# Kernel optimization log

Hardware: AMD Instinct MI355X
Metric: run time of the kernel (lower is better)

## Reference

```python
import jax, jax.numpy as jnp
import numpy as np

B, I, H, U = 2048, 512, 512, 6
NIH, IK, IV = 1, 64, 400            # input attn: heads, key/query size, value size
NCH, CK, CQ, CV = 4, 32, 32, 512    # comm attn: heads, key, query, value (CV == H required by residual add)
K = 4                               # top-k active units


def setup_inputs() -> dict:
    key = jax.random.key(0)
    ks = jax.random.split(key, 16)
    def p(k, sh, sc):
        return (sc * jax.random.normal(k, sh)).astype(jnp.float32)
    return {
        "x":  jax.random.normal(ks[0], (B, 1, I), jnp.float32),
        "hs": jax.random.normal(ks[1], (B, U, H), jnp.float32),
        "cs": jax.random.normal(ks[2], (B, U, H), jnp.float32),
        # input attention projections (nn.Linear, stored as (in,out))
        "Wk": p(ks[3], (I, NIH * IK), 0.02), "bk": jnp.zeros((NIH * IK,), jnp.float32),
        "Wv": p(ks[4], (I, NIH * IV), 0.02), "bv": jnp.zeros((NIH * IV,), jnp.float32),
        # GroupLinearLayer weights (num_blocks, din, dout), init 0.01*randn as in source
        "Wq_in": p(ks[5], (U, H, NIH * IK), 0.01),
        "Wq_c":  p(ks[6], (U, H, NCH * CQ), 0.01),
        "Wk_c":  p(ks[7], (U, H, NCH * CK), 0.01),
        "Wv_c":  p(ks[8], (U, H, NCH * CV), 0.01),
        "Wo_c":  p(ks[9], (U, NCH * CV, CV), 0.01),
        # per-unit LSTMCell params (gate order i,f,g,o)
        "W_ih": p(ks[10], (U, 4 * H, IV), 0.02),
        "W_hh": p(ks[11], (U, 4 * H, H), 0.02),
        "b_ih": jnp.zeros((U, 4 * H), jnp.float32),
        "b_hh": jnp.zeros((U, 4 * H), jnp.float32),
    }


def reference(x, hs, cs, Wk, bk, Wv, bv, Wq_in, Wq_c, Wk_c, Wv_c, Wo_c, W_ih, W_hh, b_ih, b_hh):
    b = x.shape[0]
    # append null input: (B, 2, I); column 0 = real input, column 1 = null
    x2 = jnp.concatenate([x, jnp.zeros((b, 1, I), x.dtype)], axis=1)

    # ---- input attention + top-k routing ----
    k_lay = (x2 @ Wk + bk).reshape(b, 2, NIH, IK).transpose(0, 2, 1, 3)   # (B, NIH, 2, IK)
    v_lay = (x2 @ Wv + bv).reshape(b, 2, NIH, IV).transpose(0, 2, 1, 3).mean(axis=1)  # (B, 2, IV)
    q_lay = jnp.einsum('buh,uhd->bud', hs, Wq_in).reshape(b, U, NIH, IK).transpose(0, 2, 1, 3)  # (B, NIH, U, IK)
    scores = jnp.einsum('bhud,bhnd->bhun', q_lay, k_lay) / jnp.sqrt(jnp.float32(IK))
    scores = scores.mean(axis=1)                                          # (B, U, 2)

    not_null = scores[:, :, 0]                                            # (B, U)
    _, idx = jax.lax.top_k(not_null, K)                                   # (B, K)
    mask = jnp.zeros((b, U), jnp.float32).at[jnp.arange(b)[:, None], idx].set(1.0)

    probs = jax.nn.softmax(scores, axis=-1)                               # dropout = identity (eval)
    inputs = jnp.einsum('bun,bnv->buv', probs, v_lay) * mask[:, :, None]  # (B, U, IV)

    # ---- per-unit LSTM cells (vectorized over units) ----
    gates = (jnp.einsum('buv,ugv->bug', inputs, W_ih)
             + jnp.einsum('buh,ugh->bug', hs, W_hh)
             + b_ih + b_hh)                                               # (B, U, 4H)
    i_g, f_g, g_g, o_g = jnp.split(gates, 4, axis=-1)
    c_new = jax.nn.sigmoid(f_g) * cs + jax.nn.sigmoid(i_g) * jnp.tanh(g_g)
    h_rnn = jax.nn.sigmoid(o_g) * jnp.tanh(c_new)                         # (B, U, H)

    # ---- communication attention (blocked_grad is identity in fwd) ----
    h_bg = h_rnn
    q = jnp.einsum('buh,uhd->bud', h_bg, Wq_c).reshape(b, U, NCH, CQ).transpose(0, 2, 1, 3)
    kk = jnp.einsum('buh,uhd->bud', h_bg, Wk_c).reshape(b, U, NCH, CK).transpose(0, 2, 1, 3)
    v = jnp.einsum('buh,uhd->bud', h_bg, Wv_c).reshape(b, U, NCH, CV).transpose(0, 2, 1, 3)
    att = jnp.einsum('bhud,bhnd->bhun', q, kk) / jnp.sqrt(jnp.float32(CK))  # (B, NCH, U, U)
    att = jax.nn.softmax(att, axis=-1) * mask[:, None, :, None]             # mask queries
    ctx = jnp.einsum('bhun,bhnd->bhud', att, v)                             # (B, NCH, U, CV)
    ctx = ctx.transpose(0, 2, 1, 3).reshape(b, U, NCH * CV)
    ctx = jnp.einsum('bud,udo->buo', ctx, Wo_c) + h_bg                      # residual (CV == H)

    m = mask[:, :, None]
    hs_out = m * ctx + (1.0 - m) * hs
    cs_out = m * c_new + (1.0 - m) * cs
    return (hs_out, cs_out)
```

## Files before the change

kernel.cpp:

```cpp
#include <hip/hip_runtime.h>
#include <math.h>

#define U6 6
#define BFULL 2048

typedef __bf16 bf16;
typedef __bf16 bf16x8 __attribute__((ext_vector_type(8)));
typedef float f32x4 __attribute__((ext_vector_type(4)));

__device__ __forceinline__ float sigmoidf_(float x) { return 1.0f / (1.0f + expf(-x)); }

__global__ __launch_bounds__(256) void pack_w(
    const float* __restrict__ Wk, const float* __restrict__ Wq_in,
    float* __restrict__ Wk_p, float* __restrict__ Wq_p)
{
    int idx = blockIdx.x * 256 + threadIdx.x;
    const int per = 512 * 64;
    if (idx >= 7 * per) return;
    int o = idx % per;
    int mat = idx / per;
    int j = o & 3, d = (o >> 2) & 63, kg = o >> 8;
    int k = kg * 4 + j;
    if (mat == 0) Wk_p[o] = Wk[k * 64 + d];
    else {
        int u = mat - 1;
        Wq_p[(size_t)u * per + o] = Wq_in[((size_t)u * 512 + k) * 64 + d];
    }
}

__global__ __launch_bounds__(384) void score2_kernel(
    const float* __restrict__ x, const float* __restrict__ hs,
    const float* __restrict__ Wk_p, const float* __restrict__ bk,
    const float* __restrict__ Wq_p,
    float* __restrict__ coef, float* __restrict__ maskf)
{
    __shared__ float xt[4][512];
    __shared__ float hst[4][3072];
    __shared__ float k0p[6][4][64];
    __shared__ float k0f[4][64];
    __shared__ float ss[4][6], s1s[4][6];
    const int t = threadIdx.x;
    const int u = t >> 6, d = t & 63;
    const int b4 = blockIdx.x * 4;

    for (int j = t; j < 4 * 128; j += 384)
        *(float4*)&xt[j >> 7][(j & 127) * 4] = *(const float4*)(x + (size_t)(b4 + (j >> 7)) * 512 + (j & 127) * 4);
    for (int j = t; j < 4 * 768; j += 384)
        *(float4*)&hst[j / 768][(j % 768) * 4] = *(const float4*)(hs + (size_t)(b4 + j / 768) * 3072 + (j % 768) * 4);
    __syncthreads();

    float qa[4] = {0.f, 0.f, 0.f, 0.f};
    const float4* wqp = (const float4*)(Wq_p + (size_t)u * 32768);
#pragma unroll 4
    for (int kg = 0; kg < 128; ++kg) {
        float4 w = wqp[kg * 64 + d];
#pragma unroll
        for (int b = 0; b < 4; ++b) {
            float4 h = *(const float4*)&hst[b][u * 512 + kg * 4];
            qa[b] += w.x * h.x + w.y * h.y + w.z * h.z + w.w * h.w;
        }
    }

    const int starts[6] = {0, 22, 44, 65, 86, 107};
    const int counts[6] = {22, 22, 21, 21, 21, 21};
    {
        float k0a[4] = {0.f, 0.f, 0.f, 0.f};
        const float4* wkp = (const float4*)Wk_p;
        const int st = starts[u], en = st + counts[u];
        for (int kg = st; kg < en; ++kg) {
            float4 w = wkp[kg * 64 + d];
#pragma unroll
            for (int b = 0; b < 4; ++b) {
                float4 xv = *(const float4*)&xt[b][kg * 4];
                k0a[b] += w.x * xv.x + w.y * xv.y + w.z * xv.z + w.w * xv.w;
            }
        }
#pragma unroll
        for (int b = 0; b < 4; ++b) k0p[u][b][d] = k0a[b];
    }
    __syncthreads();
    if (t < 256) {
        int b = t >> 6, dd = t & 63;
        float s = bk[dd];
#pragma unroll
        for (int uu = 0; uu < 6; ++uu) s += k0p[uu][b][dd];
        k0f[b][dd] = s;
    }
    __syncthreads();

    const float bkv = bk[d];
    float s0[4], s1[4];
#pragma unroll
    for (int b = 0; b < 4; ++b) {
        s0[b] = qa[b] * k0f[b][d];
        s1[b] = qa[b] * bkv;
    }
#pragma unroll
    for (int off = 32; off > 0; off >>= 1) {
#pragma unroll
        for (int b = 0; b < 4; ++b) {
            s0[b] += __shfl_xor(s0[b], off, 64);
            s1[b] += __shfl_xor(s1[b], off, 64);
        }
    }
    if (d == 0) {
#pragma unroll
        for (int b = 0; b < 4; ++b) { ss[b][u] = s0[b] * 0.125f; s1s[b][u] = s1[b] * 0.125f; }
    }
    __syncthreads();
    if (t < 4) {
        int bb = t;
        bool sel[6] = {false,false,false,false,false,false};
        for (int it = 0; it < 4; ++it) {
            int best = 0; float bm = -3.4e38f;
            for (int uu = 0; uu < 6; ++uu)
                if (!sel[uu] && ss[bb][uu] > bm) { bm = ss[bb][uu]; best = uu; }
            sel[best] = true;
        }
        for (int uu = 0; uu < 6; ++uu) {
            float m = sel[uu] ? 1.f : 0.f;
            float p0 = sigmoidf_(ss[bb][uu] - s1s[bb][uu]);
            maskf[(b4 + bb) * U6 + uu] = m;
            coef[(b4 + bb) * U6 + uu]  = m * p0;
        }
    }
}

__global__ __launch_bounds__(256) void build_wg(
    const float* __restrict__ Wih, const float* __restrict__ Whh,
    bf16* __restrict__ Wg)
{
    size_t idx = (size_t)blockIdx.x * 256 + threadIdx.x;
    if (idx >= 6UL * 2048 * 928) return;
    int u = (int)(idx / (2048 * 928));
    int r = (int)(idx % (2048 * 928));
    int g = r / 928, k = r - g * 928;
    float v = 0.f;
    if (k < 400)      v = Wih[((size_t)u * 2048 + g) * 400 + k];
    else if (k < 912) v = Whh[((size_t)u * 2048 + g) * 512 + (k - 400)];
    Wg[idx] = (bf16)v;
}

__global__ __launch_bounds__(256) void transpose_cvt(
    const float* __restrict__ in, bf16* __restrict__ out,
    int Kdim, int Ndim, int Nvalid, int n0base, long sInU, long sOutU)
{
    __shared__ float tile[32][33];
    const int t = threadIdx.x;
    const int c = t & 31, r8 = t >> 5;
    const int n0 = blockIdx.x * 32, k0 = blockIdx.y * 32, u = blockIdx.z;
    in  += (size_t)u * sInU;
    out += (size_t)u * sOutU;
    for (int rr = r8; rr < 32; rr += 8)
        tile[rr][c] = (n0 + c < Nvalid) ? in[(size_t)(k0 + rr) * Ndim + n0 + c] : 0.f;
    __syncthreads();
    for (int rr = r8; rr < 32; rr += 8)
        out[(size_t)(n0base + n0 + rr) * Kdim + k0 + c] = (bf16)tile[c][rr];
}

__global__ __launch_bounds__(256) void cvt16(
    const float* __restrict__ in, bf16* __restrict__ out, size_t n)
{
    size_t i = (size_t)blockIdx.x * 256 + threadIdx.x;
    if (i < n) out[i] = (bf16)in[i];
}

__global__ __launch_bounds__(256) void ag_fill(
    const float* __restrict__ hs, bf16* __restrict__ A_g)
{
    size_t idx = (size_t)blockIdx.x * 256 + threadIdx.x;
    if (idx >= (size_t)BFULL * U6 * 528) return;
    int c = (int)(idx % 528);
    size_t bu = idx / 528;
    float v = (c < 512) ? hs[bu * 512 + c] : 0.f;
    A_g[bu * 928 + 400 + c] = (bf16)v;
}

template <int EPI>
__global__ __launch_bounds__(256) void gemm_mfma(
    const bf16* __restrict__ A, int lda, long sAu,
    const bf16* __restrict__ B, long sBu,
    float* __restrict__ C, int ldc, long sCu,
    int K,
    const float* __restrict__ maskf, const float* __restrict__ hbg,
    const float* __restrict__ hs_in, float* __restrict__ out_hs, int b0)
{
    __shared__ bf16 Abuf[128 * 32];
    __shared__ bf16 Bbuf[128 * 32];
    const int t = threadIdx.x;
    const int lane = t & 63;
    const int wid = t >> 6;
    const int wr = wid >> 1, wc = wid & 1;
    const int brow0 = blockIdx.x * 128;
    const int c0 = blockIdx.y * 128;
    const int u = blockIdx.z;
    A += (size_t)u * sAu;
    B += (size_t)u * sBu;

    const int r0 = t >> 2, s0 = t & 3;
    const int r1 = r0 + 64;
    const int lo0 = r0 * 32 + ((s0 ^ ((r0 >> 1) & 3)) << 3);
    const int lo1 = r1 * 32 + ((s0 ^ ((r1 >> 1) & 3)) << 3);

    const bf16* Ap0 = A + (size_t)(brow0 + r0) * lda + s0 * 8;
    const bf16* Ap1 = A + (size_t)(brow0 + r1) * lda + s0 * 8;
    const bf16* Bp0 = B + (size_t)(c0 + r0) * K + s0 * 8;
    const bf16* Bp1 = B + (size_t)(c0 + r1) * K + s0 * 8;

    f32x4 acc[4][4];
#pragma unroll
    for (int m = 0; m < 4; ++m)
#pragma unroll
        for (int n = 0; n < 4; ++n) {
            f32x4 z = {0.f, 0.f, 0.f, 0.f};
            acc[m][n] = z;
        }

    const int nk = K >> 5;
    uint4 pa0 = *(const uint4*)(Ap0);
    uint4 pa1 = *(const uint4*)(Ap1);
    uint4 pb0 = *(const uint4*)(Bp0);
    uint4 pb1 = *(const uint4*)(Bp1);

    const int kg = lane >> 4;
    const int lr = lane & 15;

    for (int ks = 0; ks < nk; ++ks) {
        uint4 ca0 = pa0, ca1 = pa1, cb0 = pb0, cb1 = pb1;
        if (ks + 1 < nk) {
            const int kk = (ks + 1) << 5;
            pa0 = *(const uint4*)(Ap0 + kk);
            pa1 = *(const uint4*)(Ap1 + kk);
            pb0 = *(const uint4*)(Bp0 + kk);
            pb1 = *(const uint4*)(Bp1 + kk);
        }
        __syncthreads();
        *(uint4*)&Abuf[lo0] = ca0;
        *(uint4*)&Abuf[lo1] = ca1;
        *(uint4*)&Bbuf[lo0] = cb0;
        *(uint4*)&Bbuf[lo1] = cb1;
        __syncthreads();

        bf16x8 af[4], bfr[4];
#pragma unroll
        for (int m = 0; m < 4; ++m) {
            const int row = wr * 64 + m * 16 + lr;
            af[m] = *(bf16x8*)&Abuf[row * 32 + ((kg ^ ((row >> 1) & 3)) << 3)];
            const int col = wc * 64 + m * 16 + lr;
            bfr[m] = *(bf16x8*)&Bbuf[col * 32 + ((kg ^ ((col >> 1) & 3)) << 3)];
        }
#pragma unroll
        for (int m = 0; m < 4; ++m)
#pragma unroll
            for (int n = 0; n < 4; ++n)
                acc[m][n] = __builtin_amdgcn_mfma_f32_16x16x32_bf16(af[m], bfr[n], acc[m][n], 0, 0, 0);
    }

#pragma unroll
    for (int m = 0; m < 4; ++m) {
#pragma unroll
        for (int n = 0; n < 4; ++n) {
#pragma unroll
            for (int r = 0; r < 4; ++r) {
                const int row = brow0 + wr * 64 + m * 16 + kg * 4 + r;
                const int col = c0 + wc * 64 + n * 16 + lr;
                const float v = acc[m][n][r];
                if (EPI == 0) {
                    C[(size_t)u * sCu + (size_t)row * ldc + col] = v;
                } else if (EPI == 3) {
                    ((bf16*)C)[(size_t)u * sCu + (size_t)row * ldc + col] = (bf16)v;
                } else if (EPI == 2) {
                    if (col < 400) {
                        bf16* ag = (bf16*)out_hs;
                        const float bvc = hbg[col];
#pragma unroll
                        for (int uu = 0; uu < U6; ++uu) {
                            const float cf = hs_in[row * U6 + uu];
                            const float mf = maskf[row * U6 + uu];
                            ag[((size_t)row * U6 + uu) * 928 + col] = (bf16)(cf * v + mf * bvc);
                        }
                    }
                }
            }
        }
    }
}

__global__ __launch_bounds__(256) void gemm_m64_wo(
    const bf16* __restrict__ A, int lda,
    const bf16* __restrict__ B, long sBu, int K,
    const float* __restrict__ maskf, const bf16* __restrict__ h16,
    const float* __restrict__ hs_in, float* __restrict__ out_hs, int b0)
{
    __shared__ bf16 Abuf[64 * 32];
    __shared__ bf16 Bbuf[128 * 32];
    const int t = threadIdx.x;
    const int lane = t & 63;
    const int wid = t >> 6;
    const int wr = wid >> 1, wc = wid & 1;
    const int brow0 = blockIdx.x * 64;
    const int c0 = blockIdx.y * 128;
    const int u = blockIdx.z;
    B += (size_t)u * sBu;

    const int r0 = t >> 2, s0 = t & 3;
    const int r1 = r0 + 64;
    const int loA  = r0 * 32 + ((s0 ^ ((r0 >> 1) & 3)) << 3);
    const int loB0 = loA;
    const int loB1 = r1 * 32 + ((s0 ^ ((r1 >> 1) & 3)) << 3);

    const bf16* Ap  = A + (size_t)(brow0 + r0) * lda + s0 * 8;
    const bf16* Bp0 = B + (size_t)(c0 + r0) * K + s0 * 8;
    const bf16* Bp1 = B + (size_t)(c0 + r1) * K + s0 * 8;

    f32x4 acc[2][4];
#pragma unroll
    for (int m = 0; m < 2; ++m)
#pragma unroll
        for (int n = 0; n < 4; ++n) {
            f32x4 z = {0.f, 0.f, 0.f, 0.f};
            acc[m][n] = z;
        }

    const int nk = K >> 5;
    uint4 pa  = *(const uint4*)(Ap);
    uint4 pb0 = *(const uint4*)(Bp0);
    uint4 pb1 = *(const uint4*)(Bp1);

    const int kg = lane >> 4;
    const int lr = lane & 15;

    for (int ks = 0; ks < nk; ++ks) {
        uint4 ca = pa, cb0 = pb0, cb1 = pb1;
        if (ks + 1 < nk) {
            const int kk = (ks + 1) << 5;
            pa  = *(const uint4*)(Ap + kk);
            pb0 = *(const uint4*)(Bp0 + kk);
            pb1 = *(const uint4*)(Bp1 + kk);
        }
        __syncthreads();
        *(uint4*)&Abuf[loA]  = ca;
        *(uint4*)&Bbuf[loB0] = cb0;
        *(uint4*)&Bbuf[loB1] = cb1;
        __syncthreads();

        bf16x8 af[2], bfr[4];
#pragma unroll
        for (int m = 0; m < 2; ++m) {
            const int row = wr * 32 + m * 16 + lr;
            af[m] = *(bf16x8*)&Abuf[row * 32 + ((kg ^ ((row >> 1) & 3)) << 3)];
        }
#pragma unroll
        for (int n = 0; n < 4; ++n) {
            const int col = wc * 64 + n * 16 + lr;
            bfr[n] = *(bf16x8*)&Bbuf[col * 32 + ((kg ^ ((col >> 1) & 3)) << 3)];
        }
#pragma unroll
        for (int m = 0; m < 2; ++m)
#pragma unroll
            for (int n = 0; n < 4; ++n)
                acc[m][n] = __builtin_amdgcn_mfma_f32_16x16x32_bf16(af[m], bfr[n], acc[m][n], 0, 0, 0);
    }

#pragma unroll
    for (int m = 0; m < 2; ++m) {
#pragma unroll
        for (int n = 0; n < 4; ++n) {
#pragma unroll
            for (int r = 0; r < 4; ++r) {
                const int row = brow0 + wr * 32 + m * 16 + kg * 4 + r;
                const int col = c0 + wc * 64 + n * 16 + lr;
                const float mv = maskf[row * U6 + u];
                const size_t go = ((size_t)(b0 + row) * U6 + u) * 512 + col;
                out_hs[go] = (mv != 0.f)
                    ? acc[m][n][r] + (float)h16[(size_t)row * 3072 + u * 512 + col]
                    : hs_in[go];
            }
        }
    }
}

__global__ __launch_bounds__(256) void lstm_kernel(
    const float* __restrict__ gates, const float* __restrict__ b_ih,
    const float* __restrict__ b_hh, const float* __restrict__ cs,
    const float* __restrict__ maskf,
    bf16* __restrict__ h16, float* __restrict__ cs_out, int b0, int n)
{
    int idx = blockIdx.x * 256 + threadIdx.x;
    if (idx >= n) return;
    int bl = idx / 3072;
    int r = idx - bl * 3072;
    int u = r >> 9, h = r & 511;
    const float* g = gates + (size_t)bl * 12288 + u * 2048;
    int gb = u * 2048;
    float i_ = g[h]        + b_ih[gb + h]        + b_hh[gb + h];
    float f_ = g[512 + h]  + b_ih[gb + 512 + h]  + b_hh[gb + 512 + h];
    float g_ = g[1024 + h] + b_ih[gb + 1024 + h] + b_hh[gb + 1024 + h];
    float o_ = g[1536 + h] + b_ih[gb + 1536 + h] + b_hh[gb + 1536 + h];
    float c = cs[((size_t)(b0 + bl) * U6 + u) * 512 + h];
    float cn = sigmoidf_(f_) * c + sigmoidf_(i_) * tanhf(g_);
    float hv = sigmoidf_(o_) * tanhf(cn);
    h16[idx] = (bf16)hv;
    float m = maskf[bl * U6 + u];
    cs_out[((size_t)(b0 + bl) * U6 + u) * 512 + h] = (m != 0.f) ? cn : c;
}

__global__ __launch_bounds__(256) void attn_kernel(
    const bf16* __restrict__ qkv, bf16* __restrict__ ctx)
{
    const int bl = blockIdx.x, hh = blockIdx.y, t = threadIdx.x;
    __shared__ float qs[6][32], ks[6][32], att[6][8];
    if (t < 192) {
        int u = t >> 5, d = t & 31;
        const size_t rowb = (size_t)bl * 13824 + (size_t)u * 2304;
        qs[u][d] = (float)qkv[rowb + hh * 32 + d];
        ks[u][d] = (float)qkv[rowb + 128 + hh * 32 + d];
    }
    __syncthreads();
    if (t < 36) {
        int u = t / 6, n = t - (t / 6) * 6;
        float a = 0.f;
        for (int d = 0; d < 32; ++d) a += qs[u][d] * ks[n][d];
        att[u][n] = a * 0.17677669529663687f;
    }
    __syncthreads();
    if (t < 6) {
        float mx = att[t][0];
        for (int n = 1; n < 6; ++n) mx = fmaxf(mx, att[t][n]);
        float e[6], s = 0.f;
        for (int n = 0; n < 6; ++n) { e[n] = expf(att[t][n] - mx); s += e[n]; }
        for (int n = 0; n < 6; ++n) att[t][n] = e[n] / s;
    }
    __syncthreads();
    for (int e0 = t; e0 < 512; e0 += 256) {
        float vv[6];
#pragma unroll
        for (int n = 0; n < 6; ++n)
            vv[n] = (float)qkv[(size_t)bl * 13824 + (size_t)n * 2304 + 256 + hh * 512 + e0];
#pragma unroll
        for (int u = 0; u < 6; ++u) {
            float a = 0.f;
#pragma unroll
            for (int n = 0; n < 6; ++n) a += att[u][n] * vv[n];
            ctx[((size_t)bl * U6 + u) * 2048 + hh * 512 + e0] = (bf16)a;
        }
    }
}

extern "C" void kernel_launch(void* const* d_in, const int* in_sizes, int n_in,
                              void* d_out, int out_size, void* d_ws, size_t ws_size,
                              hipStream_t stream)
{
    const float* x     = (const float*)d_in[0];
    const float* hs    = (const float*)d_in[1];
    const float* cs    = (const float*)d_in[2];
    const float* Wk    = (const float*)d_in[3];
    const float* bk    = (const float*)d_in[4];
    const float* Wv    = (const float*)d_in[5];
    const float* bv    = (const float*)d_in[6];
    const float* Wq_in = (const float*)d_in[7];
    const float* Wq_c  = (const float*)d_in[8];
    const float* Wk_c  = (const float*)d_in[9];
    const float* Wv_c  = (const float*)d_in[10];
    const float* Wo_c  = (const float*)d_in[11];
    const float* W_ih  = (const float*)d_in[12];
    const float* W_hh  = (const float*)d_in[13];
    const float* b_ih  = (const float*)d_in[14];
    const float* b_hh  = (const float*)d_in[15];

    float* out_hs = (float*)d_out;
    float* out_cs = out_hs + (size_t)BFULL * U6 * 512;

    size_t off = 0;
    auto alloc = [&](size_t bytes) {
        void* p = (char*)d_ws + off;
        off = (off + bytes + 255) & ~255UL;
        return p;
    };
    bf16*  Wg    = (bf16*)alloc(6UL * 2048 * 928 * 2);
    bf16*  Wqkv  = (bf16*)alloc(6UL * 2304 * 512 * 2);
    bf16*  WoT   = (bf16*)alloc(6UL * 512 * 2048 * 2);
    bf16*  WvT   = (bf16*)alloc(512UL * 512 * 2);
    bf16*  x16   = (bf16*)alloc((size_t)BFULL * 512 * 2);
    bf16*  A_g   = (bf16*)alloc((size_t)BFULL * U6 * 928 * 2);
    float* Wk_p  = (float*)alloc(512UL * 64 * 4);
    float* Wq_p  = (float*)alloc(6UL * 512 * 64 * 4);
    float* coef  = (float*)alloc((size_t)BFULL * U6 * 4);
    float* maskf = (float*)alloc((size_t)BFULL * U6 * 4);
    const size_t fixedB = off;

    const size_t perRow = 52224 + 6144;
    int NC = 1;
    while (NC < 16 && fixedB + (size_t)(BFULL / NC) * perRow + 4096 > ws_size) NC *= 2;
    const int Bc = BFULL / NC;

    char*  R1    = (char*)alloc((size_t)Bc * 52224);
    bf16*  h16   = (bf16*)alloc((size_t)Bc * 6144);

    float* gates = (float*)R1;
    bf16*  qkv16 = (bf16*)R1;
    bf16*  ctx16 = (bf16*)(R1 + (size_t)Bc * 27648);

    {
        size_t n = 6UL * 2048 * 928;
        build_wg<<<(int)((n + 255) / 256), 256, 0, stream>>>(W_ih, W_hh, Wg);
    }
    transpose_cvt<<<dim3(4, 16, U6), 256, 0, stream>>>(Wq_c, Wqkv, 512, 128, 128, 0,
                                                       512L * 128, 2304L * 512);
    transpose_cvt<<<dim3(4, 16, U6), 256, 0, stream>>>(Wk_c, Wqkv, 512, 128, 128, 128,
                                                       512L * 128, 2304L * 512);
    transpose_cvt<<<dim3(64, 16, U6), 256, 0, stream>>>(Wv_c, Wqkv, 512, 2048, 2048, 256,
                                                        512L * 2048, 2304L * 512);
    transpose_cvt<<<dim3(16, 64, U6), 256, 0, stream>>>(Wo_c, WoT, 2048, 512, 512, 0,
                                                        2048L * 512, 512L * 2048);
    transpose_cvt<<<dim3(16, 16, 1), 256, 0, stream>>>(Wv, WvT, 512, 400, 400, 0, 0, 0);
    pack_w<<<(7 * 512 * 64 + 255) / 256, 256, 0, stream>>>(Wk, Wq_in, Wk_p, Wq_p);
    cvt16<<<(int)(((size_t)BFULL * 512 + 255) / 256), 256, 0, stream>>>(
        x, x16, (size_t)BFULL * 512);
    score2_kernel<<<BFULL / 4, 384, 0, stream>>>(x, hs, Wk_p, bk, Wq_p, coef, maskf);
    gemm_mfma<2><<<dim3(BFULL / 128, 4, 1), 256, 0, stream>>>(
        x16, 512, 0L, WvT, 0L, nullptr, 0, 0L, 512,
        maskf, bv, coef, (float*)A_g, 0);
    ag_fill<<<(int)(((size_t)BFULL * U6 * 528 + 255) / 256), 256, 0, stream>>>(hs, A_g);

    for (int c = 0; c < NC; ++c) {
        const int b0 = c * Bc;
        gemm_mfma<0><<<dim3(Bc / 128, 16, U6), 256, 0, stream>>>(
            A_g + (size_t)b0 * 5568, 5568, 928L, Wg, 2048L * 928,
            gates, 12288, 2048L, 928,
            nullptr, nullptr, nullptr, nullptr, 0);
        {
            int n = Bc * 3072;
            lstm_kernel<<<(n + 255) / 256, 256, 0, stream>>>(
                gates, b_ih, b_hh, cs, maskf + (size_t)b0 * U6, h16, out_cs, b0, n);
        }
        gemm_mfma<3><<<dim3(Bc / 128, 18, U6), 256, 0, stream>>>(
            h16, 3072, 512L, Wqkv, 2304L * 512, (float*)qkv16, 13824, 2304L, 512,
            nullptr, nullptr, nullptr, nullptr, 0);
        attn_kernel<<<dim3(Bc, 4), 256, 0, stream>>>(qkv16, ctx16);
        gemm_m64_wo<<<dim3(Bc / 64, 4, U6), 256, 0, stream>>>(
            ctx16, 2048, WoT, 512L * 2048, 2048,
            maskf + (size_t)b0 * U6, h16, hs, out_hs, b0);
    }
}
```

Baseline: 575.2 us.

## Fuse LSTM cell into gate GEMM epilogue with interleaved gates and folded bias

Gate weight rows are reordered so each 128-column tile holds all four gates of 32 hidden units. The LSTM nonlinearity then runs in the GEMM epilogue through shared memory, which removes the fp32 gates buffer write and read and a separate kernel launch. Biases are folded into the GEMM as an extra K column, with a ones column added to A. A workgroup index swizzle across 8 groups is also added to the GEMM kernels to improve cache locality. The cost is a heavier epilogue with extra syncs, and the bias now passes through bf16.

```diff
diff --git a/kernel.cpp b/kernel.cpp
--- a/kernel.cpp
+++ b/kernel.cpp
@@ -9,6 +9,17 @@
 typedef float f32x4 __attribute__((ext_vector_type(4)));
 
 __device__ __forceinline__ float sigmoidf_(float x) { return 1.0f / (1.0f + expf(-x)); }
+
+__device__ __forceinline__ void swz_block(int& bx, int& by, int& bz) {
+    const int nx = gridDim.x, ny = gridDim.y, nz = gridDim.z;
+    const int nwg = nx * ny * nz;
+    int lin = blockIdx.x + nx * (blockIdx.y + ny * blockIdx.z);
+    if ((nwg & 7) == 0) {
+        const int cpx = nwg >> 3;
+        lin = (lin & 7) * cpx + (lin >> 3);
+    }
+    bx = lin % nx; int tq = lin / nx; by = tq % ny; bz = tq / ny;
+}
 
 __global__ __launch_bounds__(256) void pack_w(
     const float* __restrict__ Wk, const float* __restrict__ Wq_in,
@@ -128,16 +139,20 @@
 
 __global__ __launch_bounds__(256) void build_wg(
     const float* __restrict__ Wih, const float* __restrict__ Whh,
+    const float* __restrict__ bih, const float* __restrict__ bhh,
     bf16* __restrict__ Wg)
 {
     size_t idx = (size_t)blockIdx.x * 256 + threadIdx.x;
     if (idx >= 6UL * 2048 * 928) return;
     int u = (int)(idx / (2048 * 928));
     int r = (int)(idx % (2048 * 928));
-    int g = r / 928, k = r - g * 928;
+    int gp = r / 928, k = r - gp * 928;
+    int h = gp >> 2, gate = gp & 3;
+    int gsrc = gate * 512 + h;
     float v = 0.f;
-    if (k < 400)      v = Wih[((size_t)u * 2048 + g) * 400 + k];
-    else if (k < 912) v = Whh[((size_t)u * 2048 + g) * 512 + (k - 400)];
+    if (k < 400)       v = Wih[((size_t)u * 2048 + gsrc) * 400 + k];
+    else if (k < 912)  v = Whh[((size_t)u * 2048 + gsrc) * 512 + (k - 400)];
+    else if (k == 912) v = bih[(size_t)u * 2048 + gsrc] + bhh[(size_t)u * 2048 + gsrc];
     Wg[idx] = (bf16)v;
 }
 
@@ -172,7 +187,7 @@
     if (idx >= (size_t)BFULL * U6 * 528) return;
     int c = (int)(idx % 528);
     size_t bu = idx / 528;
-    float v = (c < 512) ? hs[bu * 512 + c] : 0.f;
+    float v = (c < 512) ? hs[bu * 512 + c] : ((c == 512) ? 1.0f : 0.f);
     A_g[bu * 928 + 400 + c] = (bf16)v;
 }
 
@@ -187,13 +202,15 @@
 {
     __shared__ bf16 Abuf[128 * 32];
     __shared__ bf16 Bbuf[128 * 32];
+    int bxi, byi, bzi;
+    swz_block(bxi, byi, bzi);
     const int t = threadIdx.x;
     const int lane = t & 63;
     const int wid = t >> 6;
     const int wr = wid >> 1, wc = wid & 1;
-    const int brow0 = blockIdx.x * 128;
-    const int c0 = blockIdx.y * 128;
-    const int u = blockIdx.z;
+    const int brow0 = bxi * 128;
+    const int c0 = byi * 128;
+    const int u = bzi;
     A += (size_t)u * sAu;
     B += (size_t)u * sBu;
 
@@ -265,9 +282,7 @@
                 const int row = brow0 + wr * 64 + m * 16 + kg * 4 + r;
                 const int col = c0 + wc * 64 + n * 16 + lr;
                 const float v = acc[m][n][r];
-                if (EPI == 0) {
-                    C[(size_t)u * sCu + (size_t)row * ldc + col] = v;
-                } else if (EPI == 3) {
+                if (EPI == 3) {
                     ((bf16*)C)[(size_t)u * sCu + (size_t)row * ldc + col] = (bf16)v;
                 } else if (EPI == 2) {
                     if (col < 400) {
@@ -286,6 +301,123 @@
     }
 }
 
+__global__ __launch_bounds__(256) void gemm_gates_fused(
+    const bf16* __restrict__ A,
+    const bf16* __restrict__ Wg,
+    const float* __restrict__ cs,
+    const float* __restrict__ maskf,
+    bf16* __restrict__ h16,
+    float* __restrict__ cs_out,
+    int b0)
+{
+    __shared__ bf16 smem[2 * 128 * 32];
+    bf16* Abuf = smem;
+    bf16* Bbuf = smem + 128 * 32;
+    int bxi, byi, bzi;
+    swz_block(bxi, byi, bzi);
+    const int t = threadIdx.x;
+    const int lane = t & 63;
+    const int wid = t >> 6;
+    const int wr = wid >> 1, wc = wid & 1;
+    const int brow0 = bxi * 128;
+    const int c0 = byi * 128;
+    const int u = bzi;
+    const bf16* Au = A + (size_t)u * 928;
+    const bf16* Bu = Wg + (size_t)u * 2048 * 928;
+    const int K = 928;
+
+    const int r0 = t >> 2, s0 = t & 3;
+    const int r1 = r0 + 64;
+    const int lo0 = r0 * 32 + ((s0 ^ ((r0 >> 1) & 3)) << 3);
+    const int lo1 = r1 * 32 + ((s0 ^ ((r1 >> 1) & 3)) << 3);
+
+    const bf16* Ap0 = Au + (size_t)(brow0 + r0) * 5568 + s0 * 8;
+    const bf16* Ap1 = Au + (size_t)(brow0 + r1) * 5568 + s0 * 8;
+    const bf16* Bp0 = Bu + (size_t)(c0 + r0) * K + s0 * 8;
+    const bf16* Bp1 = Bu + (size_t)(c0 + r1) * K + s0 * 8;
+
+    f32x4 acc[4][4];
+#pragma unroll
+    for (int m = 0; m < 4; ++m)
+#pragma unroll
+        for (int n = 0; n < 4; ++n) {
+            f32x4 z = {0.f, 0.f, 0.f, 0.f};
+            acc[m][n] = z;
+        }
+
+    const int nk = K >> 5;
+    uint4 pa0 = *(const uint4*)(Ap0);
+    uint4 pa1 = *(const uint4*)(Ap1);
+    uint4 pb0 = *(const uint4*)(Bp0);
+    uint4 pb1 = *(const uint4*)(Bp1);
+
+    const int kg = lane >> 4;
+    const int lr = lane & 15;
+
+    for (int ks = 0; ks < nk; ++ks) {
+        uint4 ca0 = pa0, ca1 = pa1, cb0 = pb0, cb1 = pb1;
+        if (ks + 1 < nk) {
+            const int kk = (ks + 1) << 5;
+            pa0 = *(const uint4*)(Ap0 + kk);
+            pa1 = *(const uint4*)(Ap1 + kk);
+            pb0 = *(const uint4*)(Bp0 + kk);
+            pb1 = *(const uint4*)(Bp1 + kk);
+        }
+        __syncthreads();
+        *(uint4*)&Abuf[lo0] = ca0;
+        *(uint4*)&Abuf[lo1] = ca1;
+        *(uint4*)&Bbuf[lo0] = cb0;
+        *(uint4*)&Bbuf[lo1] = cb1;
+        __syncthreads();
+
+        bf16x8 af[4], bfr[4];
+#pragma unroll
+        for (int m = 0; m < 4; ++m) {
+            const int row = wr * 64 + m * 16 + lr;
+            af[m] = *(bf16x8*)&Abuf[row * 32 + ((kg ^ ((row >> 1) & 3)) << 3)];
+            const int col = wc * 64 + m * 16 + lr;
+            bfr[m] = *(bf16x8*)&Bbuf[col * 32 + ((kg ^ ((col >> 1) & 3)) << 3)];
+        }
+#pragma unroll
+        for (int m = 0; m < 4; ++m)
+#pragma unroll
+            for (int n = 0; n < 4; ++n)
+                acc[m][n] = __builtin_amdgcn_mfma_f32_16x16x32_bf16(af[m], bfr[n], acc[m][n], 0, 0, 0);
+    }
+
+    float* st = (float*)smem;
+    const int hbase = c0 >> 2;
+#pragma unroll
+    for (int m = 0; m < 4; ++m) {
+        __syncthreads();
+#pragma unroll
+        for (int n = 0; n < 4; ++n) {
+#pragma unroll
+            for (int r = 0; r < 4; ++r) {
+                const int lrow = wr * 16 + kg * 4 + r;
+                const int col  = wc * 64 + n * 16 + lr;
+                st[lrow * 128 + col] = acc[m][n][r];
+            }
+        }
+        __syncthreads();
+#pragma unroll
+        for (int i = 0; i < 4; ++i) {
+            const int p = i * 256 + t;
+            const int hl = p & 31, lrow = p >> 5;
+            const int grow = brow0 + (lrow >> 4) * 64 + m * 16 + (lrow & 15);
+            const int hg = hbase + hl;
+            const float4 g4 = *(const float4*)&st[lrow * 128 + hl * 4];
+            const size_t cidx = ((size_t)(b0 + grow) * U6 + u) * 512 + hg;
+            const float c = cs[cidx];
+            const float cn = sigmoidf_(g4.y) * c + sigmoidf_(g4.x) * tanhf(g4.z);
+            const float hv = sigmoidf_(g4.w) * tanhf(cn);
+            h16[(size_t)grow * 3072 + u * 512 + hg] = (bf16)hv;
+            const float mk = maskf[grow * U6 + u];
+            cs_out[cidx] = (mk != 0.f) ? cn : c;
+        }
+    }
+}
+
 __global__ __launch_bounds__(256) void gemm_m64_wo(
     const bf16* __restrict__ A, int lda,
     const bf16* __restrict__ B, long sBu, int K,
@@ -294,13 +426,15 @@
 {
     __shared__ bf16 Abuf[64 * 32];
     __shared__ bf16 Bbuf[128 * 32];
+    int bxi, byi, bzi;
+    swz_block(bxi, byi, bzi);
     const int t = threadIdx.x;
     const int lane = t & 63;
     const int wid = t >> 6;
     const int wr = wid >> 1, wc = wid & 1;
-    const int brow0 = blockIdx.x * 64;
-    const int c0 = blockIdx.y * 128;
-    const int u = blockIdx.z;
+    const int brow0 = bxi * 64;
+    const int c0 = byi * 128;
+    const int u = bzi;
     B += (size_t)u * sBu;
 
     const int r0 = t >> 2, s0 = t & 3;
@@ -378,31 +512,6 @@
             }
         }
     }
-}
-
-__global__ __launch_bounds__(256) void lstm_kernel(
-    const float* __restrict__ gates, const float* __restrict__ b_ih,
-    const float* __restrict__ b_hh, const float* __restrict__ cs,
-    const float* __restrict__ maskf,
-    bf16* __restrict__ h16, float* __restrict__ cs_out, int b0, int n)
-{
-    int idx = blockIdx.x * 256 + threadIdx.x;
-    if (idx >= n) return;
-    int bl = idx / 3072;
-    int r = idx - bl * 3072;
-    int u = r >> 9, h = r & 511;
-    const float* g = gates + (size_t)bl * 12288 + u * 2048;
-    int gb = u * 2048;
-    float i_ = g[h]        + b_ih[gb + h]        + b_hh[gb + h];
-    float f_ = g[512 + h]  + b_ih[gb + 512 + h]  + b_hh[gb + 512 + h];
-    float g_ = g[1024 + h] + b_ih[gb + 1024 + h] + b_hh[gb + 1024 + h];
-    float o_ = g[1536 + h] + b_ih[gb + 1536 + h] + b_hh[gb + 1536 + h];
-    float c = cs[((size_t)(b0 + bl) * U6 + u) * 512 + h];
-    float cn = sigmoidf_(f_) * c + sigmoidf_(i_) * tanhf(g_);
-    float hv = sigmoidf_(o_) * tanhf(cn);
-    h16[idx] = (bf16)hv;
-    float m = maskf[bl * U6 + u];
-    cs_out[((size_t)(b0 + bl) * U6 + u) * 512 + h] = (m != 0.f) ? cn : c;
 }
 
 __global__ __launch_bounds__(256) void attn_kernel(
@@ -497,13 +606,12 @@
     char*  R1    = (char*)alloc((size_t)Bc * 52224);
     bf16*  h16   = (bf16*)alloc((size_t)Bc * 6144);
 
-    float* gates = (float*)R1;
     bf16*  qkv16 = (bf16*)R1;
     bf16*  ctx16 = (bf16*)(R1 + (size_t)Bc * 27648);
 
     {
         size_t n = 6UL * 2048 * 928;
-        build_wg<<<(int)((n + 255) / 256), 256, 0, stream>>>(W_ih, W_hh, Wg);
+        build_wg<<<(int)((n + 255) / 256), 256, 0, stream>>>(W_ih, W_hh, b_ih, b_hh, Wg);
     }
     transpose_cvt<<<dim3(4, 16, U6), 256, 0, stream>>>(Wq_c, Wqkv, 512, 128, 128, 0,
                                                        512L * 128, 2304L * 512);
@@ -525,15 +633,9 @@
 
     for (int c = 0; c < NC; ++c) {
         const int b0 = c * Bc;
-        gemm_mfma<0><<<dim3(Bc / 128, 16, U6), 256, 0, stream>>>(
-            A_g + (size_t)b0 * 5568, 5568, 928L, Wg, 2048L * 928,
-            gates, 12288, 2048L, 928,
-            nullptr, nullptr, nullptr, nullptr, 0);
-        {
-            int n = Bc * 3072;
-            lstm_kernel<<<(n + 255) / 256, 256, 0, stream>>>(
-                gates, b_ih, b_hh, cs, maskf + (size_t)b0 * U6, h16, out_cs, b0, n);
-        }
+        gemm_gates_fused<<<dim3(Bc / 128, 16, U6), 256, 0, stream>>>(
+            A_g + (size_t)b0 * 5568, Wg, cs, maskf + (size_t)b0 * U6,
+            h16, out_cs, b0);
         gemm_mfma<3><<<dim3(Bc / 128, 18, U6), 256, 0, stream>>>(
             h16, 3072, 512L, Wqkv, 2304L * 512, (float*)qkv16, 13824, 2304L, 512,
             nullptr, nullptr, nullptr, nullptr, 0);
```

Result: faster. 545.8 us (-5.1%).
